# Kernel optimization log

Hardware: AMD Instinct MI355X
Metric: run time of the kernel (lower is better)

The kernel has to match this reference:

```python
import jax, jax.numpy as jnp
import numpy as np

IN_SIZE = 224
KERNEL = 5
STRIDE = 1
IN_CH = 16
OUT_CH = 64
LAMB = 5.0
LR = 0.005
GAMMA = 0.99
EPS_ = 0.01
NH = (IN_SIZE - KERNEL) // STRIDE + 1          # 220 output positions per side
NB_TILES = NH * NH                              # 48400 tiles


def setup_inputs() -> dict:
    key = jax.random.key(0)
    k1, k2 = jax.random.split(key)
    x = jax.random.normal(k1, (1, IN_CH, IN_SIZE, IN_SIZE), dtype=jnp.float32)
    # torch.nn.init.uniform_(param, a=0, b=1)
    W = jax.random.uniform(k2, (OUT_CH, IN_CH, KERNEL, KERNEL), dtype=jnp.float32)
    exp_avg = jnp.zeros((OUT_CH,), dtype=jnp.float32)
    return {"x": x, "W": W, "exp_avg": exp_avg, "clamped": 0}


def _inhibition(out):
    out = jax.nn.relu(out)
    m = jnp.max(out, axis=1, keepdims=True)     # max over channel dim
    out = out / (m + 1e-9)
    return out ** LAMB


def _flatten_input(x):
    # mirrors x.unfold(2,k,s).unfold(3,k,s) -> [T, C*k*k] with (C, kh, kw) ordering
    starts = jnp.arange(NH) * STRIDE
    rows = starts[:, None] + jnp.arange(KERNEL)  # [NH, K]
    p = x[0][:, rows]                            # [C, NH, K, W]
    p = p[:, :, :, rows]                         # [C, NH, K, NH, K]
    p = p.transpose(1, 3, 0, 2, 4)               # [NH, NH, C, K, K]
    return p.reshape(NB_TILES, -1)               # [T, D]


def reference(x, W, exp_avg, clamped):
    # forward conv + inhibition
    out = jax.lax.conv_general_dilated(
        x, W, (STRIDE, STRIDE), 'VALID',
        dimension_numbers=('NCHW', 'OIHW', 'NCHW'))
    out = _inhibition(out)                       # [1, O, NH, NH]

    # Hebbian FullyOrthogonal update (no-grad buffer update in the original)
    y = out[0].transpose(1, 2, 0).reshape(-1, OUT_CH)   # [T, O]
    xf = _flatten_input(x)                               # [T, D]
    Wf = W.reshape(OUT_CH, -1)                           # [O, D]
    # mean_t( lr * (y_t (x) x_t - y_t (x) (y_t W)) ) = lr/T * (Y^T X - (Y^T Y) W)
    yty = y.T @ y                                        # [O, O]
    avg_delta = (LR / NB_TILES) * (y.T @ xf - yty @ Wf)  # [O, D]
    Wnew = jax.nn.relu(Wf + avg_delta).reshape(OUT_CH, IN_CH, KERNEL, KERNEL)
    exp_new = GAMMA * exp_avg + (1.0 - GAMMA) * jnp.mean(y, axis=0)

    # weight decay scaling
    A = exp_new / jnp.mean(exp_new)
    gfp = EPS_ * jnp.tanh(-EPS_ * (A - 1.0)) + 1.0
    gfn = 1.0 / gfp
    pos = jnp.where(Wnew > 0, Wnew, 0.0) * gfp.reshape(-1, 1, 1, 1)
    neg = jnp.where(Wnew < 0, Wnew, 0.0) * gfn.reshape(-1, 1, 1, 1)
    Wfinal = pos + neg
    return out, Wfinal, exp_new
```

## Files before the change

kernel.cpp:

```cpp
#include <hip/hip_runtime.h>
#include <stdint.h>

#define IN_SIZE 224
#define KER 5
#define IN_CH 16
#define OUT_CH 64
#define NH 220
#define NB_TILES (NH * NH)
#define XCH (IN_SIZE * IN_SIZE)
#define OUT_PLANE NB_TILES
#define KP2 51200
#define XS 52224
#define XTROWS 50304
#define LR_OVER_NB ((float)(0.005 / 48400.0))
#define GAMMA_F 0.99f
#define ONE_MINUS_GAMMA 0.01f
#define EPS_F 0.01f

#define NCHUNK 64
#define CK 800
#define PSTRIDE (64 * 512)

typedef __attribute__((ext_vector_type(8))) short short8;
typedef __attribute__((ext_vector_type(4))) float floatx4;

__device__ inline uint16_t f2bf(float f) {
    uint32_t u = __float_as_uint(f);
    return (uint16_t)((u + 0x7FFFu + ((u >> 16) & 1u)) >> 16);
}
__device__ inline float bf2f(uint16_t h) { return __uint_as_float((uint32_t)h << 16); }

__global__ __launch_bounds__(256) void prep_kernel(const float* __restrict__ x,
                                                   uint16_t* __restrict__ xs,
                                                   uint16_t* __restrict__ yb,
                                                   uint16_t* __restrict__ ones,
                                                   uint16_t* __restrict__ xth,
                                                   uint16_t* __restrict__ xtl,
                                                   const float* __restrict__ W,
                                                   uint16_t* __restrict__ wrh,
                                                   uint16_t* __restrict__ wrl) {
    int blk = blockIdx.x;
    if (blk < 4080) {
        int t = blk * 256 + threadIdx.x;
        const int perq = XS / 4;
        if (t < 5 * 16 * perq) {
            int kj = t / (16 * perq);
            int rem = t - kj * (16 * perq);
            int c = rem / perq;
            int q = (rem - c * perq) * 4;
            int base = c * XCH;
            ushort4 o;
            int i0 = q + kj;     o.x = f2bf(x[base + (i0 < XCH ? i0 : XCH - 1)]);
            int i1 = q + kj + 1; o.y = f2bf(x[base + (i1 < XCH ? i1 : XCH - 1)]);
            int i2 = q + kj + 2; o.z = f2bf(x[base + (i2 < XCH ? i2 : XCH - 1)]);
            int i3 = q + kj + 3; o.w = f2bf(x[base + (i3 < XCH ? i3 : XCH - 1)]);
            *(ushort4*)(xs + (kj * 16 + c) * XS + q) = o;
        }
        ushort4 z = {0, 0, 0, 0};
        if (t < 64 * 480) {
            int r = t / 480, q = (t - r * 480) * 4;
            *(ushort4*)(yb + r * KP2 + 49280 + q) = z;
        }
        if (t < 64 * 220) {
            int o = t / 220, i = t - o * 220;
            *(ushort4*)(yb + o * KP2 + i * 224 + 220) = z;
        }
        if (t < 12816) {
            ushort4 o1 = {0x3F80, 0x3F80, 0x3F80, 0x3F80};
            ((ushort4*)ones)[t] = o1;
        }
    } else if (blk < 4080 + 197) {
        int addr = (blk - 4080) * 256 + threadIdx.x;
        if (addr >= XTROWS) return;
        uint32_t dh[8], dl[8];
        if (addr < XCH) {
#pragma unroll
            for (int q = 0; q < 8; q++) {
                float v0 = x[(2 * q) * XCH + addr];
                float v1 = x[(2 * q + 1) * XCH + addr];
                uint16_t h0 = f2bf(v0), h1 = f2bf(v1);
                uint16_t l0 = f2bf(v0 - bf2f(h0)), l1 = f2bf(v1 - bf2f(h1));
                dh[q] = (uint32_t)h0 | ((uint32_t)h1 << 16);
                dl[q] = (uint32_t)l0 | ((uint32_t)l1 << 16);
            }
        } else {
#pragma unroll
            for (int q = 0; q < 8; q++) { dh[q] = 0u; dl[q] = 0u; }
        }
        *(uint4*)(xth + addr * 16) = make_uint4(dh[0], dh[1], dh[2], dh[3]);
        *(uint4*)(xth + addr * 16 + 8) = make_uint4(dh[4], dh[5], dh[6], dh[7]);
        *(uint4*)(xtl + addr * 16) = make_uint4(dl[0], dl[1], dl[2], dl[3]);
        *(uint4*)(xtl + addr * 16 + 8) = make_uint4(dl[4], dl[5], dl[6], dl[7]);
    } else {
        int idx = (blk - 4080 - 197) * 256 + threadIdx.x;
        if (idx >= 13 * 4 * 64 * 8) return;
        int j = idx & 7;
        int lane = (idx >> 3) & 63;
        int ocg = (idx >> 9) & 3;
        int t = idx >> 11;
        int k = (lane >> 4) * 8 + j;
        int s = k >> 4, c = k & 15;
        int oc = 16 * ocg + (lane & 15);
        int tap = 2 * t + s;
        float v = (tap < 25) ? W[oc * 400 + c * 25 + tap] : 0.f;
        uint16_t h = f2bf(v);
        wrh[idx] = h;
        wrl[idx] = f2bf(v - bf2f(h));
    }
}

__global__ __launch_bounds__(256) void conv_inhib_kernel(const uint16_t* __restrict__ xth,
                                                         const uint16_t* __restrict__ xtl,
                                                         const uint16_t* __restrict__ wrh,
                                                         const uint16_t* __restrict__ wrl,
                                                         float* __restrict__ out,
                                                         uint16_t* __restrict__ yb) {
    const int lane = threadIdx.x & 63;
    const int w = threadIdx.x >> 6;
    const int l15 = lane & 15;
    const int quad = lane >> 4;
    const int P0 = blockIdx.x * 64;
    const int c0 = (quad & 1) * 8;
    const int sq = quad >> 1;

    floatx4 acc[4];
#pragma unroll
    for (int g = 0; g < 4; g++) acc[g] = (floatx4){0.f, 0.f, 0.f, 0.f};

#pragma unroll
    for (int t = 0; t < 13; t++) {
        short8 ah = *(const short8*)(wrh + ((t * 4 + w) * 64 + lane) * 8);
        short8 al = *(const short8*)(wrl + ((t * 4 + w) * 64 + lane) * 8);
        const int tap0 = 2 * t, tap1 = 2 * t + 1;
        const int o0 = (tap0 / 5) * 224 + (tap0 % 5);
        const int o1 = (tap1 <= 24) ? (tap1 / 5) * 224 + (tap1 % 5) : 0;
        const int off = sq ? o1 : o0;
#pragma unroll
        for (int g = 0; g < 4; g++) {
            int P = P0 + 16 * g + l15;
            short8 bh = *(const short8*)(xth + (P + off) * 16 + c0);
            short8 bl = *(const short8*)(xtl + (P + off) * 16 + c0);
            acc[g] = __builtin_amdgcn_mfma_f32_16x16x32_bf16(ah, bh, acc[g], 0, 0, 0);
            acc[g] = __builtin_amdgcn_mfma_f32_16x16x32_bf16(ah, bl, acc[g], 0, 0, 0);
            acc[g] = __builtin_amdgcn_mfma_f32_16x16x32_bf16(al, bh, acc[g], 0, 0, 0);
        }
    }

    __shared__ float wmax[4][64];
    float pmax[4];
#pragma unroll
    for (int g = 0; g < 4; g++) {
        float mx = fmaxf(fmaxf(acc[g][0], acc[g][1]), fmaxf(acc[g][2], acc[g][3]));
        mx = fmaxf(mx, 0.f);
        mx = fmaxf(mx, __shfl_xor(mx, 16));
        mx = fmaxf(mx, __shfl_xor(mx, 32));
        pmax[g] = mx;
    }
    if (quad == 0) {
#pragma unroll
        for (int g = 0; g < 4; g++) wmax[w][g * 16 + l15] = pmax[g];
    }
    __syncthreads();

#pragma unroll
    for (int g = 0; g < 4; g++) {
        int P = P0 + 16 * g + l15;
        int i = P / 224;
        int j = P - i * 224;
        bool valid = j < NH;
        float mx = fmaxf(fmaxf(wmax[0][g * 16 + l15], wmax[1][g * 16 + l15]),
                         fmaxf(wmax[2][g * 16 + l15], wmax[3][g * 16 + l15]));
        float inv = 1.f / (mx + 1e-9f);
#pragma unroll
        for (int r = 0; r < 4; r++) {
            float tv = fmaxf(acc[g][r], 0.f) * inv;
            float t2 = tv * tv;
            tv = t2 * t2 * tv;
            if (valid) {
                int oc = 16 * w + quad * 4 + r;
                out[oc * OUT_PLANE + i * NH + j] = tv;
                yb[oc * KP2 + P] = f2bf(tv);
            }
        }
    }
}

__global__ __launch_bounds__(256) void gemm_kernel(const uint16_t* __restrict__ yb,
                                                   const uint16_t* __restrict__ xs,
                                                   const uint16_t* __restrict__ ones,
                                                   float* __restrict__ Mpart) {
    __shared__ uint16_t As[2][64 * 40];
    __shared__ uint16_t Bs[2][64 * 40];
    const int tid = threadIdx.x;
    const int lane = tid & 63;
    const int w = tid >> 6;
    const int l15 = lane & 15;
    const int quad = lane >> 4;
    const int kg = quad * 8;
    const int b = blockIdx.x;
    const int xcd = b & 7;
    const int t8 = b >> 3;
    const int ntile = t8 & 7;
    const int chunk = xcd + 8 * (t8 >> 3);
    const int k0 = chunk * CK;

    const int sr = tid >> 2;
    const int sseg = (tid & 3) * 8;
    const uint16_t* pa = yb + sr * KP2 + k0 + sseg;

    int n_g = ntile * 64 + sr;
    const uint16_t* pbase;
    if (n_g < 400) {
        int c = n_g / 25;
        int r = n_g - 25 * c;
        int ki = r / 5;
        int kj = r - 5 * ki;
        pbase = xs + (kj * 16 + c) * XS + ki * 224;
    } else if (n_g < 464) {
        pbase = yb + (n_g - 400) * KP2;
    } else if (n_g == 464) {
        pbase = ones;
    } else {
        pbase = yb;
    }
    const uint16_t* pb = pbase + k0 + sseg;

    floatx4 acc[4];
#pragma unroll
    for (int i = 0; i < 4; i++) acc[i] = (floatx4){0.f, 0.f, 0.f, 0.f};

    uint4 ra = *(const uint4*)pa;
    uint4 rb = *(const uint4*)pb;

    for (int s = 0; s < 25; s++) {
        const int p = s & 1;
        *(uint4*)&As[p][sr * 40 + sseg] = ra;
        *(uint4*)&Bs[p][sr * 40 + sseg] = rb;
        __syncthreads();
        if (s + 1 < 25) {
            pa += 32;
            pb += 32;
            ra = *(const uint4*)pa;
            rb = *(const uint4*)pb;
        }
        short8 af = *(const short8*)&As[p][(16 * w + l15) * 40 + kg];
#pragma unroll
        for (int ng = 0; ng < 4; ng++) {
            short8 bf = *(const short8*)&Bs[p][(16 * ng + l15) * 40 + kg];
            acc[ng] = __builtin_amdgcn_mfma_f32_16x16x32_bf16(af, bf, acc[ng], 0, 0, 0);
        }
        __syncthreads();
    }

    float* dst = Mpart + chunk * PSTRIDE;
#pragma unroll
    for (int ng = 0; ng < 4; ng++) {
        int col = ntile * 64 + ng * 16 + l15;
        if (col < 465) {
#pragma unroll
            for (int r = 0; r < 4; r++)
                dst[(16 * w + quad * 4 + r) * 512 + col] = acc[ng][r];
        }
    }
}

__global__ __launch_bounds__(256) void finalize_w_kernel(const float* __restrict__ W,
                                                         const float* __restrict__ Mpart,
                                                         const float* __restrict__ exp_avg,
                                                         float* __restrict__ Wout,
                                                         float* __restrict__ expout) {
    __shared__ float gfps[OUT_CH];
    __shared__ float ytys[2][OUT_CH];
    const int tid = threadIdx.x;
    const int bid = blockIdx.x;
    const int first_o = (bid * 256) / 400;

    if (tid < OUT_CH) {
        int o = tid;
        float cs = 0.f;
#pragma unroll 8
        for (int ch = 0; ch < NCHUNK; ch++) cs += Mpart[ch * PSTRIDE + o * 512 + 464];
        float e = GAMMA_F * exp_avg[o] + ONE_MINUS_GAMMA * (cs / (float)NB_TILES);
        float s = e;
        for (int off = 32; off; off >>= 1) s += __shfl_down(s, off);
        s = __shfl(s, 0);
        float A = e / (s / (float)OUT_CH);
        gfps[o] = EPS_F * tanhf(-EPS_F * (A - 1.f)) + 1.f;
        if (bid == 0) expout[o] = e;
    }
    if (tid >= 128) {
        int t = tid - 128;
        int orow = first_o + (t >> 6);
        int k = t & 63;
        float s = 0.f;
        if (orow < OUT_CH) {
#pragma unroll 8
            for (int ch = 0; ch < NCHUNK; ch++) s += Mpart[ch * PSTRIDE + orow * 512 + 400 + k];
        }
        ytys[t >> 6][k] = s;
    }
    __syncthreads();

    int idx = bid * 256 + tid;
    int o = idx / 400;
    int q = idx - o * 400;
    float Mv = 0.f;
#pragma unroll 8
    for (int ch = 0; ch < NCHUNK; ch++) Mv += Mpart[ch * PSTRIDE + o * 512 + q];
    const float* yrow = ytys[o - first_o];
    float dot = 0.f;
#pragma unroll 8
    for (int k = 0; k < OUT_CH; k++) dot = fmaf(yrow[k], W[k * 400 + q], dot);
    float wv = W[idx] + LR_OVER_NB * (Mv - dot);
    wv = fmaxf(wv, 0.f);
    float gp = gfps[o];
    float pos = (wv > 0.f ? wv : 0.f) * gp;
    float neg = (wv < 0.f ? wv : 0.f) / gp;
    Wout[idx] = pos + neg;
}

extern "C" void kernel_launch(void* const* d_in, const int* in_sizes, int n_in,
                              void* d_out, int out_size, void* d_ws, size_t ws_size,
                              hipStream_t stream) {
    const float* x = (const float*)d_in[0];
    const float* W = (const float*)d_in[1];
    const float* exp_avg = (const float*)d_in[2];
    float* out = (float*)d_out;

    float* wsf = (float*)d_ws;
    float* Mpart = wsf + 29760;
    uint16_t* xth = (uint16_t*)Mpart;
    uint16_t* xtl = xth + XTROWS * 16;
    uint16_t* wrh = xtl + XTROWS * 16;
    uint16_t* wrl = wrh + 26624;
    uint16_t* ybf = (uint16_t*)(wsf + 29760 + NCHUNK * PSTRIDE);
    uint16_t* xsb = ybf + OUT_CH * KP2;
    uint16_t* ones = xsb + 5 * 16 * XS;

    float* Wout = out + OUT_CH * OUT_PLANE;
    float* expout = Wout + OUT_CH * IN_CH * KER * KER;

    prep_kernel<<<4080 + 197 + 104, 256, 0, stream>>>(x, xsb, ybf, ones, xth, xtl, W, wrh, wrl);
    conv_inhib_kernel<<<770, 256, 0, stream>>>(xth, xtl, wrh, wrl, out, ybf);
    gemm_kernel<<<512, 256, 0, stream>>>(ybf, xsb, ones, Mpart);
    finalize_w_kernel<<<100, 256, 0, stream>>>(W, Mpart, exp_avg, Wout, expout);
}
```

Baseline: 119.1 us.

## Replace 5x column-shifted bf16 copies of x with one copy and in-register shifting

The prep kernel used to write five column-shifted bf16 copies of the input (one per kernel column offset), about 8 MB of writes. It now converts x to a single bf16 copy plus zero padding. The GEMM B-tile loader reads 8 extra bytes per row and applies a funnel shift in registers to recover the kj offset. This removes most of the prep kernel's memory traffic and blocks, at the cost of extra loads and ALU shift work in the GEMM load path.

```diff
diff --git a/kernel.cpp b/kernel.cpp
--- a/kernel.cpp
+++ b/kernel.cpp
@@ -10,8 +10,8 @@
 #define XCH (IN_SIZE * IN_SIZE)
 #define OUT_PLANE NB_TILES
 #define KP2 51200
-#define XS 52224
 #define XTROWS 50304
+#define XCPAD 2048
 #define LR_OVER_NB ((float)(0.005 / 48400.0))
 #define GAMMA_F 0.99f
 #define ONE_MINUS_GAMMA 0.01f
@@ -31,7 +31,7 @@
 __device__ inline float bf2f(uint16_t h) { return __uint_as_float((uint32_t)h << 16); }
 
 __global__ __launch_bounds__(256) void prep_kernel(const float* __restrict__ x,
-                                                   uint16_t* __restrict__ xs,
+                                                   uint16_t* __restrict__ xc,
                                                    uint16_t* __restrict__ yb,
                                                    uint16_t* __restrict__ ones,
                                                    uint16_t* __restrict__ xth,
@@ -40,23 +40,18 @@
                                                    uint16_t* __restrict__ wrh,
                                                    uint16_t* __restrict__ wrl) {
     int blk = blockIdx.x;
-    if (blk < 4080) {
+    if (blk < 784) {
         int t = blk * 256 + threadIdx.x;
-        const int perq = XS / 4;
-        if (t < 5 * 16 * perq) {
-            int kj = t / (16 * perq);
-            int rem = t - kj * (16 * perq);
-            int c = rem / perq;
-            int q = (rem - c * perq) * 4;
-            int base = c * XCH;
+        if (t < 16 * XCH / 4) {
+            float4 v = ((const float4*)x)[t];
             ushort4 o;
-            int i0 = q + kj;     o.x = f2bf(x[base + (i0 < XCH ? i0 : XCH - 1)]);
-            int i1 = q + kj + 1; o.y = f2bf(x[base + (i1 < XCH ? i1 : XCH - 1)]);
-            int i2 = q + kj + 2; o.z = f2bf(x[base + (i2 < XCH ? i2 : XCH - 1)]);
-            int i3 = q + kj + 3; o.w = f2bf(x[base + (i3 < XCH ? i3 : XCH - 1)]);
-            *(ushort4*)(xs + (kj * 16 + c) * XS + q) = o;
+            o.x = f2bf(v.x); o.y = f2bf(v.y); o.z = f2bf(v.z); o.w = f2bf(v.w);
+            ((ushort4*)xc)[t] = o;
         }
         ushort4 z = {0, 0, 0, 0};
+        if (t < XCPAD / 4) {
+            ((ushort4*)(xc + 16 * XCH))[t] = z;
+        }
         if (t < 64 * 480) {
             int r = t / 480, q = (t - r * 480) * 4;
             *(ushort4*)(yb + r * KP2 + 49280 + q) = z;
@@ -69,8 +64,8 @@
             ushort4 o1 = {0x3F80, 0x3F80, 0x3F80, 0x3F80};
             ((ushort4*)ones)[t] = o1;
         }
-    } else if (blk < 4080 + 197) {
-        int addr = (blk - 4080) * 256 + threadIdx.x;
+    } else if (blk < 784 + 197) {
+        int addr = (blk - 784) * 256 + threadIdx.x;
         if (addr >= XTROWS) return;
         uint32_t dh[8], dl[8];
         if (addr < XCH) {
@@ -92,7 +87,7 @@
         *(uint4*)(xtl + addr * 16) = make_uint4(dl[0], dl[1], dl[2], dl[3]);
         *(uint4*)(xtl + addr * 16 + 8) = make_uint4(dl[4], dl[5], dl[6], dl[7]);
     } else {
-        int idx = (blk - 4080 - 197) * 256 + threadIdx.x;
+        int idx = (blk - 784 - 197) * 256 + threadIdx.x;
         if (idx >= 13 * 4 * 64 * 8) return;
         int j = idx & 7;
         int lane = (idx >> 3) & 63;
@@ -186,7 +181,7 @@
 }
 
 __global__ __launch_bounds__(256) void gemm_kernel(const uint16_t* __restrict__ yb,
-                                                   const uint16_t* __restrict__ xs,
+                                                   const uint16_t* __restrict__ xc,
                                                    const uint16_t* __restrict__ ones,
                                                    float* __restrict__ Mpart) {
     __shared__ uint16_t As[2][64 * 40];
@@ -210,12 +205,15 @@
 
     int n_g = ntile * 64 + sr;
     const uint16_t* pbase;
+    int fidx = 0, fsh = 0;
     if (n_g < 400) {
         int c = n_g / 25;
         int r = n_g - 25 * c;
         int ki = r / 5;
         int kj = r - 5 * ki;
-        pbase = xs + (kj * 16 + c) * XS + ki * 224;
+        pbase = xc + c * XCH + ki * 224;
+        fidx = kj >> 1;
+        fsh = (kj & 1) * 16;
     } else if (n_g < 464) {
         pbase = yb + (n_g - 400) * KP2;
     } else if (n_g == 464) {
@@ -231,17 +229,29 @@
 
     uint4 ra = *(const uint4*)pa;
     uint4 rb = *(const uint4*)pb;
+    uint2 rbx = *(const uint2*)(pb + 8);
 
     for (int s = 0; s < 25; s++) {
         const int p = s & 1;
         *(uint4*)&As[p][sr * 40 + sseg] = ra;
-        *(uint4*)&Bs[p][sr * 40 + sseg] = rb;
+        {
+            uint32_t dw[7];
+            *(uint4*)dw = rb;
+            *(uint2*)(dw + 4) = rbx;
+            dw[6] = 0u;
+            uint32_t bo[4];
+#pragma unroll
+            for (int t = 0; t < 4; t++)
+                bo[t] = (uint32_t)((((uint64_t)dw[fidx + t + 1] << 32) | dw[fidx + t]) >> fsh);
+            *(uint4*)&Bs[p][sr * 40 + sseg] = *(uint4*)bo;
+        }
         __syncthreads();
         if (s + 1 < 25) {
             pa += 32;
             pb += 32;
             ra = *(const uint4*)pa;
             rb = *(const uint4*)pb;
+            rbx = *(const uint2*)(pb + 8);
         }
         short8 af = *(const short8*)&As[p][(16 * w + l15) * 40 + kg];
 #pragma unroll
@@ -334,14 +344,14 @@
     uint16_t* wrh = xtl + XTROWS * 16;
     uint16_t* wrl = wrh + 26624;
     uint16_t* ybf = (uint16_t*)(wsf + 29760 + NCHUNK * PSTRIDE);
-    uint16_t* xsb = ybf + OUT_CH * KP2;
-    uint16_t* ones = xsb + 5 * 16 * XS;
+    uint16_t* xcb = ybf + OUT_CH * KP2;
+    uint16_t* ones = xcb + 16 * XCH + XCPAD;
 
     float* Wout = out + OUT_CH * OUT_PLANE;
     float* expout = Wout + OUT_CH * IN_CH * KER * KER;
 
-    prep_kernel<<<4080 + 197 + 104, 256, 0, stream>>>(x, xsb, ybf, ones, xth, xtl, W, wrh, wrl);
+    prep_kernel<<<784 + 197 + 104, 256, 0, stream>>>(x, xcb, ybf, ones, xth, xtl, W, wrh, wrl);
     conv_inhib_kernel<<<770, 256, 0, stream>>>(xth, xtl, wrh, wrl, out, ybf);
-    gemm_kernel<<<512, 256, 0, stream>>>(ybf, xsb, ones, Mpart);
+    gemm_kernel<<<512, 256, 0, stream>>>(ybf, xcb, ones, Mpart);
     finalize_w_kernel<<<100, 256, 0, stream>>>(W, Mpart, exp_avg, Wout, expout);
 }
```

Measured after the change: 124.1 us. +4.2%, slower.
